# Kernel tuning notes

Hardware: AMD Instinct MI355X
Metric: run time of the kernel (lower is better)

## Reference

```python
import jax, jax.numpy as jnp
import numpy as np

V, S, D, H, L = 32000, 2048, 768, 12, 6
HD = D // H
EPS = 1e-5


def _sinusoidal_pe(s, d):
    pos = np.arange(s)[:, None].astype(np.float32)
    div = np.exp(np.arange(0, d, 2).astype(np.float32) * (-np.log(10000.0) / d))
    pe = np.zeros((s, d), dtype=np.float32)
    pe[:, 0::2] = np.sin(pos * div)
    pe[:, 1::2] = np.cos(pos * div)
    return jnp.asarray(pe)


def setup_inputs() -> dict:
    key = jax.random.key(0)
    ks = jax.random.split(key, 16)
    std = 0.02
    tok_emb = jax.random.normal(ks[0], (V, D), jnp.float32) * std
    tok_emb = tok_emb.at[1].set(0.0)  # padding_idx=1
    pos_enc = _sinusoidal_pe(S, D)
    attn_w = jax.random.normal(ks[1], (L, 3 * D, D), jnp.float32) * std
    attn_b = jnp.zeros((L, 3 * D), jnp.float32)
    proj_std = 0.02 / np.sqrt(2 * 6)
    proj_w = jax.random.normal(ks[2], (L, D, D), jnp.float32) * proj_std
    proj_b = jnp.zeros((L, D), jnp.float32)
    ln1_g = jnp.ones((L, D), jnp.float32); ln1_b = jnp.zeros((L, D), jnp.float32)
    ln2_g = jnp.ones((L, D), jnp.float32); ln2_b = jnp.zeros((L, D), jnp.float32)
    fc1_w = jax.random.normal(ks[3], (L, 4 * D, D), jnp.float32) * std
    fc1_b = jnp.zeros((L, 4 * D), jnp.float32)
    fc2_w = jax.random.normal(ks[4], (L, D, 4 * D), jnp.float32) * std
    fc2_b = jnp.zeros((L, D), jnp.float32)
    dec_w = jax.random.normal(ks[5], (V, D), jnp.float32) * std
    idx = jax.random.randint(ks[6], (2, S), 0, V)
    return dict(idx=idx, tok_emb=tok_emb, pos_enc=pos_enc, attn_w=attn_w,
                attn_b=attn_b, proj_w=proj_w, proj_b=proj_b, ln1_g=ln1_g,
                ln1_b=ln1_b, ln2_g=ln2_g, ln2_b=ln2_b, fc1_w=fc1_w,
                fc1_b=fc1_b, fc2_w=fc2_w, fc2_b=fc2_b, dec_w=dec_w)


def _ln(x, g, b):
    mu = jnp.mean(x, -1, keepdims=True)
    var = jnp.mean(jnp.square(x - mu), -1, keepdims=True)
    return (x - mu) * jax.lax.rsqrt(var + EPS) * g + b


def _forward(idx, tok_emb, pos_enc, attn_w, attn_b, proj_w, proj_b,
             ln1_g, ln1_b, ln2_g, ln2_b, fc1_w, fc1_b, fc2_w, fc2_b, dec_w):
    b, s = idx.shape
    x = tok_emb[idx] + pos_enc[:s]  # [b,s,d]
    for l in range(L):
        h = _ln(x, ln1_g[l], ln1_b[l])
        qkv = h @ attn_w[l].T + attn_b[l]
        q, k, v = jnp.split(qkv, 3, axis=-1)
        q = q.reshape(b, s, H, HD).transpose(0, 2, 1, 3)
        k = k.reshape(b, s, H, HD).transpose(0, 2, 1, 3)
        v = v.reshape(b, s, H, HD).transpose(0, 2, 1, 3)
        att = jnp.einsum('bhqd,bhkd->bhqk', q, k) * (1.0 / np.sqrt(HD))
        att = jax.nn.softmax(att, axis=-1)  # no causal mask in source
        y = jnp.einsum('bhqk,bhkd->bhqd', att, v)
        y = y.transpose(0, 2, 1, 3).reshape(b, s, D)
        x = x + (y @ proj_w[l].T + proj_b[l])
        h = _ln(x, ln2_g[l], ln2_b[l])
        h = jax.nn.gelu(h @ fc1_w[l].T + fc1_b[l])
        x = x + (h @ fc2_w[l].T + fc2_b[l])
    return x @ dec_w.T  # [b,s,V]


def reference(idx, tok_emb, pos_enc, attn_w, attn_b, proj_w, proj_b,
              ln1_g, ln1_b, ln2_g, ln2_b, fc1_w, fc1_b, fc2_w, fc2_b, dec_w):
    return _forward(idx, tok_emb, pos_enc, attn_w, attn_b, proj_w, proj_b,
                    ln1_g, ln1_b, ln2_g, ln2_b, fc1_w, fc1_b, fc2_w, fc2_b, dec_w)
```

## Files before the change

kernel.cpp:

```cpp
#include <hip/hip_runtime.h>
#include <hip/hip_bf16.h>
#include <stdint.h>


typedef unsigned short u16;
typedef __attribute__((ext_vector_type(8))) __bf16 bf16x8;
typedef __attribute__((ext_vector_type(4))) float f32x4;
typedef __attribute__((ext_vector_type(4))) unsigned int u32x4;
typedef __attribute__((ext_vector_type(4))) unsigned short u16x4;
typedef __attribute__((ext_vector_type(8))) unsigned short u16x8;

#define MFMA16(a, b, c) __builtin_amdgcn_mfma_f32_16x16x32_bf16((a), (b), (c), 0, 0, 0)

__device__ __forceinline__ float b2f(u16 u) {
  union { unsigned int i; float f; } x; x.i = ((unsigned int)u) << 16; return x.f;
}
__device__ __forceinline__ u16 f2b(float f) {
  union { float f; unsigned int i; } x; x.f = f;
  unsigned int r = x.i + 0x7fffu + ((x.i >> 16) & 1u);
  return (u16)(r >> 16);
}
__device__ __forceinline__ unsigned int cvtpk(float lo, float hi) {
  unsigned int r;
  asm("v_cvt_pk_bf16_f32 %0, %1, %2" : "=v"(r) : "v"(lo), "v"(hi));
  return r;
}
__device__ __forceinline__ float gelu_f(float v) {
  const float t = 0.7978845608028654f * (v + 0.044715f * v * v * v);
  const float e = __expf(-2.f * fabsf(t));
  float th = (1.f - e) / (1.f + e);
  th = (t < 0.f) ? -th : th;
  return 0.5f * v * (1.f + th);
}
__device__ __forceinline__ void lds16(u16* l, const u16* g) {
  __builtin_amdgcn_global_load_lds(
      (const __attribute__((address_space(1))) unsigned int*)g,
      (__attribute__((address_space(3))) unsigned int*)l, 16, 0, 0);
}

__global__ __launch_bounds__(256) void conv5_kernel(
    const float* __restrict__ s0, u16* __restrict__ d0, int n0,
    const float* __restrict__ s1, u16* __restrict__ d1, int n1,
    const float* __restrict__ s2, u16* __restrict__ d2, int n2,
    const float* __restrict__ s3, u16* __restrict__ d3, int n3,
    const float* __restrict__ s4, u16* __restrict__ d4, int n4) {
  const float* src; u16* dst; int n8;
  switch (blockIdx.y) {
    case 0: src = s0; dst = d0; n8 = n0; break;
    case 1: src = s1; dst = d1; n8 = n1; break;
    case 2: src = s2; dst = d2; n8 = n2; break;
    case 3: src = s3; dst = d3; n8 = n3; break;
    default: src = s4; dst = d4; n8 = n4; break;
  }
  int i = blockIdx.x * 256 + threadIdx.x;
  const int stride = gridDim.x * 256;
  for (; i < n8; i += stride) {
    const f32x4 a = *(const f32x4*)&src[(size_t)i * 8];
    const f32x4 b = *(const f32x4*)&src[(size_t)i * 8 + 4];
    u16x8 p;
#pragma unroll
    for (int j = 0; j < 4; ++j) { p[j] = f2b(a[j]); p[4 + j] = f2b(b[j]); }
    *(u16x8*)&dst[(size_t)i * 8] = p;
  }
}

__global__ __launch_bounds__(256) void convh_kernel(
    const float* __restrict__ src, u16* __restrict__ dst) {
  const int i = blockIdx.x * 256 + threadIdx.x;
  const f32x4 a = *(const f32x4*)&src[(size_t)i * 8];
  const f32x4 b = *(const f32x4*)&src[(size_t)i * 8 + 4];
  u16x8 p;
#pragma unroll
  for (int j = 0; j < 4; ++j) { p[j] = f2b(a[j]); p[4 + j] = f2b(b[j]); }
  *(u16x8*)&dst[(size_t)i * 8] = p;
}

__global__ __launch_bounds__(256) void embed_kernel(
    const int* __restrict__ idx, const float* __restrict__ tok,
    const float* __restrict__ pos, float* __restrict__ x) {
  const int t = blockIdx.x;
  const int s = t & 2047;
  const int tid = threadIdx.x;
  const size_t to = (size_t)idx[t] * 768;
  const size_t po = (size_t)s * 768;
  float* xr = x + (size_t)t * 768;
#pragma unroll
  for (int i = 0; i < 3; ++i) {
    const int d = tid + i * 256;
    xr[d] = tok[to + d] + pos[po + d];
  }
}

__global__ __launch_bounds__(256) void ln_kernel(
    const float* __restrict__ x, const float* __restrict__ g,
    const float* __restrict__ b, u16* __restrict__ out) {
  const int w = threadIdx.x >> 6, lane = threadIdx.x & 63;
  const int row = blockIdx.x * 4 + w;
  const float* xr = x + (size_t)row * 768;
  f32x4 v[3];
#pragma unroll
  for (int i = 0; i < 3; ++i) v[i] = *(const f32x4*)&xr[i * 256 + lane * 4];
  float s = 0.f;
#pragma unroll
  for (int i = 0; i < 3; ++i)
#pragma unroll
    for (int j = 0; j < 4; ++j) s += v[i][j];
#pragma unroll
  for (int m = 1; m < 64; m <<= 1) s += __shfl_xor(s, m);
  const float mu = s * (1.f / 768.f);
  float q = 0.f;
#pragma unroll
  for (int i = 0; i < 3; ++i)
#pragma unroll
    for (int j = 0; j < 4; ++j) {
      const float d = v[i][j] - mu;
      q += d * d;
    }
#pragma unroll
  for (int m = 1; m < 64; m <<= 1) q += __shfl_xor(q, m);
  const float rs = rsqrtf(q * (1.f / 768.f) + 1e-5f);
  u16* orow = out + (size_t)row * 768;
#pragma unroll
  for (int i = 0; i < 3; ++i) {
    const f32x4 gg = *(const f32x4*)&g[i * 256 + lane * 4];
    const f32x4 bb = *(const f32x4*)&b[i * 256 + lane * 4];
    u16x4 o;
#pragma unroll
    for (int j = 0; j < 4; ++j) o[j] = f2b((v[i][j] - mu) * rs * gg[j] + bb[j]);
    *(u16x4*)&orow[i * 256 + lane * 4] = o;
  }
}

template <int MODE, int MFAST, int SPLITK>
__global__ __launch_bounds__(256) void gemm_bb(
    const u16* __restrict__ A, const u16* __restrict__ B,
    const float* __restrict__ bias, u16* __restrict__ outb,
    float* __restrict__ outf, float* __restrict__ resid,
    u16* __restrict__ mirror, int N, int K) {
  __shared__ alignas(16) u16 As[2][128 * 64];
  __shared__ alignas(16) u16 Bs[2][128 * 64];
  const int tid = threadIdx.x;
  const int lane = tid & 63;
  const int w = tid >> 6;
  const int wr = (w >> 1) * 64;
  const int wc = (w & 1) * 64;
  const int fr = lane & 15;
  const int fg = lane >> 4;
  const int bn0 = (MFAST ? blockIdx.y : blockIdx.x) * 128;
  const int bm0 = (MFAST ? blockIdx.x : blockIdx.y) * 128;
  const int srow = tid >> 3;
  const int kseg = K / SPLITK;
  const int kbeg = (SPLITK > 1) ? blockIdx.z * kseg : 0;
  const int kend = kbeg + kseg;

  f32x4 acc[4][4] = {};

  auto stage = [&](int buf, int bk0) {
#pragma unroll
    for (int i = 0; i < 4; ++i) {
      const int row = i * 32 + srow;
      const int slot = (tid & 7) ^ (row & 7);
      lds16(&As[buf][(i * 256 + w * 64) * 8],
            &A[(size_t)(bm0 + row) * K + bk0 + slot * 8]);
      lds16(&Bs[buf][(i * 256 + w * 64) * 8],
            &B[(size_t)(bn0 + row) * K + bk0 + slot * 8]);
    }
  };

  stage(0, kbeg);
  int cur = 0;
  for (int bk0 = kbeg; bk0 < kend; bk0 += 64) {
    __syncthreads();
    if (bk0 + 64 < kend) stage(cur ^ 1, bk0 + 64);
#pragma unroll
    for (int kk = 0; kk < 64; kk += 32) {
      bf16x8 af[4], bfv[4];
#pragma unroll
      for (int m = 0; m < 4; ++m) {
        const int row = wr + m * 16 + fr;
        const int slot = ((kk >> 3) + fg) ^ (row & 7);
        af[m] = *(const bf16x8*)&As[cur][row * 64 + slot * 8];
      }
#pragma unroll
      for (int n = 0; n < 4; ++n) {
        const int row = wc + n * 16 + fr;
        const int slot = ((kk >> 3) + fg) ^ (row & 7);
        bfv[n] = *(const bf16x8*)&Bs[cur][row * 64 + slot * 8];
      }
#pragma unroll
      for (int m = 0; m < 4; ++m)
#pragma unroll
        for (int n = 0; n < 4; ++n)
          acc[m][n] = MFMA16(af[m], bfv[n], acc[m][n]);
    }
    cur ^= 1;
  }

  if (MODE == 4 && bn0 >= 1536) {
#pragma unroll
    for (int n = 0; n < 4; ++n) {
      const int col = bn0 + wc + n * 16 + fr;
      const float bv = bias[col];
      const int hcol = col - 1536;
      const size_t vbase =
          (size_t)(hcol >> 6) * 64 * 2048 + (size_t)(hcol & 63) * 2048;
#pragma unroll
      for (int m = 0; m < 4; ++m) {
        const int row0 = bm0 + wr + m * 16 + fg * 4;
        const size_t bboff = (size_t)(row0 >> 11) * 12 * 64 * 2048;
        const int s = row0 & 2047;
        u16x4 o;
#pragma unroll
        for (int r = 0; r < 4; ++r) o[r] = f2b(acc[m][n][r] + bv);
        *(u16x4*)&mirror[bboff + vbase + s] = o;
      }
    }
    return;
  }

#pragma unroll
  for (int n = 0; n < 4; ++n) {
    const int col = bn0 + wc + n * 16 + fr;
    const float bv =
        (bias && (SPLITK == 1 || blockIdx.z == 0)) ? bias[col] : 0.0f;
#pragma unroll
    for (int m = 0; m < 4; ++m) {
#pragma unroll
      for (int r = 0; r < 4; ++r) {
        const int row = bm0 + wr + m * 16 + fg * 4 + r;
        float v = acc[m][n][r] + bv;
        if (MODE == 1) v = gelu_f(v);
        const size_t off = (size_t)row * N + col;
        if (MODE == 2) {
          const float nv = resid[off] + v;
          resid[off] = nv;
          if (mirror) mirror[off] = f2b(nv);
        } else if (MODE == 5) {
          atomicAdd(&resid[off], v);
        } else if (MODE == 3) {
          __builtin_nontemporal_store(v, &outf[off]);
        } else {
          outb[off] = f2b(v);
        }
      }
    }
  }
}

#define G8PHASE(H, MH, LOADB)                                                 \
  {                                                                           \
    if (LOADB) {                                                              \
      _Pragma("unroll") for (int n = 0; n < 4; ++n) {                         \
        const int row = wn * 64 + n * 16 + fr;                                \
        bfv[n] = *(const bf16x8*)&Bs_[bufr * 16384 + (H) * 8192 + row * 32 +  \
                                      ((fg ^ ((row ^ (row >> 2)) & 3)) << 3)];\
      }                                                                       \
    }                                                                         \
    bf16x8 af[4];                                                             \
    _Pragma("unroll") for (int m = 0; m < 4; ++m) {                           \
      const int row = wm * 128 + (MH) * 64 + m * 16 + fr;                     \
      af[m] = *(const bf16x8*)&As_[bufr * 16384 + (H) * 8192 + row * 32 +     \
                                   ((fg ^ ((row ^ (row >> 2)) & 3)) << 3)];   \
    }                                                                         \
    __builtin_amdgcn_s_setprio(1);                                            \
    _Pragma("unroll") for (int m = 0; m < 4; ++m)                             \
      _Pragma("unroll") for (int n = 0; n < 4; ++n)                           \
        acc[(MH) * 4 + m][n] = MFMA16(af[m], bfv[n], acc[(MH) * 4 + m][n]);   \
    __builtin_amdgcn_s_setprio(0);                                            \
  }

template <int MODE, int MFAST>
__global__ __launch_bounds__(512, 2) void gemm8(
    const u16* __restrict__ A, const u16* __restrict__ B,
    const float* __restrict__ bias, u16* __restrict__ outb,
    float* __restrict__ outf, float* __restrict__ resid, int N, int K) {
  extern __shared__ u16 sm8[];
  u16* As_ = sm8;
  u16* Bs_ = sm8 + 32768;
  const int tid = threadIdx.x;
  const int lane = tid & 63;
  const int w = tid >> 6;
  const int wm = w >> 2;
  const int wn = w & 3;
  const int fr = lane & 15;
  const int fg = lane >> 4;
  const int bn0 = (MFAST ? blockIdx.y : blockIdx.x) * 256;
  const int bm0 = (MFAST ? blockIdx.x : blockIdx.y) * 256;
  const int nt = K >> 6;

  f32x4 acc[8][4] = {};
  bf16x8 bfv[4];

  auto stage = [&](u16* lbase, const u16* __restrict__ M, int rbase, int k0) {
#pragma unroll
    for (int i = 0; i < 2; ++i) {
      const int c = i * 512 + tid;
      const int row = c >> 2;
      const int slot = (c & 3) ^ ((row ^ (row >> 2)) & 3);
      lds16(lbase + (i * 512 + w * 64) * 8,
            M + (size_t)(rbase + row) * K + k0 + slot * 8);
    }
  };

  stage(As_ + 0, A, bm0, 0);
  stage(Bs_ + 0, B, bn0, 0);
  stage(As_ + 8192, A, bm0, 32);
  stage(Bs_ + 8192, B, bn0, 32);

  int bufr = 0;
  for (int t = 0; t < nt; ++t) {
    const int tn = (t + 1 < nt) ? t + 1 : t;
    const int bufw = bufr ^ 1;
    const int kn = tn * 64;
    asm volatile("s_waitcnt vmcnt(4)" ::: "memory");
    __builtin_amdgcn_sched_barrier(0);
    __builtin_amdgcn_s_barrier();
    stage(As_ + bufw * 16384, A, bm0, kn);
    G8PHASE(0, 0, true)
    stage(Bs_ + bufw * 16384, B, bn0, kn);
    G8PHASE(0, 1, false)
    asm volatile("s_waitcnt vmcnt(4)" ::: "memory");
    __builtin_amdgcn_sched_barrier(0);
    __builtin_amdgcn_s_barrier();
    stage(As_ + bufw * 16384 + 8192, A, bm0, kn + 32);
    G8PHASE(1, 0, true)
    stage(Bs_ + bufw * 16384 + 8192, B, bn0, kn + 32);
    G8PHASE(1, 1, false)
    bufr ^= 1;
  }

#pragma unroll
  for (int n = 0; n < 4; ++n) {
    const int col = bn0 + wn * 64 + n * 16 + fr;
    const float bv = bias ? bias[col] : 0.0f;
#pragma unroll
    for (int i = 0; i < 8; ++i) {
#pragma unroll
      for (int r = 0; r < 4; ++r) {
        const int row = bm0 + wm * 128 + i * 16 + fg * 4 + r;
        float v = acc[i][n][r] + bv;
        if (MODE == 1) v = gelu_f(v);
        const size_t off = (size_t)row * N + col;
        if (MODE == 2) {
          resid[off] += v;
        } else if (MODE == 3) {
          __builtin_nontemporal_store(v, &outf[off]);
        } else {
          outb[off] = f2b(v);
        }
      }
    }
  }
}

template <int MODE>
__global__ __launch_bounds__(256) void gemm_bt(
    const u16* __restrict__ A, const float* __restrict__ B,
    const float* __restrict__ bias, u16* __restrict__ outb,
    float* __restrict__ outf, float* __restrict__ resid,
    u16* __restrict__ mirror, int N, int K) {
  __shared__ alignas(16) u16 As[128 * 64];
  __shared__ alignas(16) u16 Bs[128 * 64];
  const int tid = threadIdx.x;
  const int lane = tid & 63;
  const int w = tid >> 6;
  const int wr = (w >> 1) * 64;
  const int wc = (w & 1) * 64;
  const int fr = lane & 15;
  const int fg = lane >> 4;
  const int bn0 = blockIdx.x * 128;
  const int bm0 = blockIdx.y * 128;

  f32x4 acc[4][4] = {};

  for (int bk0 = 0; bk0 < K; bk0 += 64) {
    __syncthreads();
#pragma unroll
    for (int i = 0; i < 4; ++i) {
      const int c = i * 256 + tid;
      const int row = c >> 3;
      const int e0 = (c & 7) * 8;
      *(u32x4*)&As[row * 64 + e0] =
          *(const u32x4*)&A[(size_t)(bm0 + row) * K + bk0 + e0];
    }
#pragma unroll
    for (int i = 0; i < 8; ++i) {
      const int c = i * 256 + tid;
      const int row = c >> 4;
      const int e0 = (c & 15) * 4;
      const f32x4 fv = *(const f32x4*)&B[(size_t)(bn0 + row) * K + bk0 + e0];
      u16x4 pv;
#pragma unroll
      for (int j = 0; j < 4; ++j) pv[j] = f2b(fv[j]);
      *(u16x4*)&Bs[row * 64 + e0] = pv;
    }
    __syncthreads();
#pragma unroll
    for (int kk = 0; kk < 64; kk += 32) {
      bf16x8 af[4], bfv[4];
#pragma unroll
      for (int m = 0; m < 4; ++m)
        af[m] = *(const bf16x8*)&As[(wr + m * 16 + fr) * 64 + kk + fg * 8];
#pragma unroll
      for (int n = 0; n < 4; ++n)
        bfv[n] = *(const bf16x8*)&Bs[(wc + n * 16 + fr) * 64 + kk + fg * 8];
#pragma unroll
      for (int m = 0; m < 4; ++m)
#pragma unroll
        for (int n = 0; n < 4; ++n)
          acc[m][n] = MFMA16(af[m], bfv[n], acc[m][n]);
    }
  }

#pragma unroll
  for (int n = 0; n < 4; ++n) {
    const int col = bn0 + wc + n * 16 + fr;
    const float bv = bias ? bias[col] : 0.0f;
#pragma unroll
    for (int m = 0; m < 4; ++m) {
#pragma unroll
      for (int r = 0; r < 4; ++r) {
        const int row = bm0 + wr + m * 16 + fg * 4 + r;
        float v = acc[m][n][r] + bv;
        if (MODE == 1) v = gelu_f(v);
        const size_t off = (size_t)row * N + col;
        if (MODE == 2) {
          const float nv = resid[off] + v;
          resid[off] = nv;
          if (mirror) mirror[off] = f2b(nv);
        } else if (MODE == 3) {
          __builtin_nontemporal_store(v, &outf[off]);
        } else {
          outb[off] = f2b(v);
        }
      }
    }
  }
}

__global__ __launch_bounds__(256) void vtrans_kernel(
    const u16* __restrict__ qkv, u16* __restrict__ vt) {
  __shared__ u16 tile[64][72];
  const int tid = threadIdx.x;
  const int s0 = blockIdx.x * 64;
  const int hh = blockIdx.y;
  const int bb = blockIdx.z;
  const size_t tb = (size_t)bb * 2048 * 2304;
#pragma unroll
  for (int i = 0; i < 2; ++i) {
    const int c = i * 256 + tid;
    const int sl = c >> 3;
    const int d0 = (c & 7) * 8;
    *(u16x8*)&tile[sl][d0] =
        *(const u16x8*)&qkv[tb + (size_t)(s0 + sl) * 2304 + 1536 + hh * 64 + d0];
  }
  __syncthreads();
  const size_t vtb = (size_t)((bb * 12 + hh) * 64) * 2048;
#pragma unroll
  for (int i = 0; i < 2; ++i) {
    const int c = i * 256 + tid;
    const int d = c >> 3;
    const int so = (c & 7) * 8;
    u16x8 p;
#pragma unroll
    for (int j = 0; j < 8; ++j) p[j] = tile[so + j][d];
    *(u16x8*)&vt[vtb + (size_t)d * 2048 + s0 + so] = p;
  }
}

__global__ __launch_bounds__(256) void attn_kernel(
    const u16* __restrict__ qkv, const u16* __restrict__ vt,
    u16* __restrict__ y) {
  __shared__ alignas(16) u16 Ks[2][64 * 64];
  __shared__ alignas(16) u16 VTs[2][64 * 64];
  __shared__ alignas(16) u16 Ps[4][16 * 64];
  const int tid = threadIdx.x;
  const int lane = tid & 63;
  const int w = tid >> 6;
  const int fr = lane & 15;
  const int fg = lane >> 4;
  const int hh = blockIdx.y;
  const int bb = blockIdx.z;
  const size_t tb = (size_t)bb * 2048 * 2304;
  const size_t vtb = (size_t)((bb * 12 + hh) * 64) * 2048;
  const int q0 = blockIdx.x * 64 + w * 16;

  const bf16x8 qf0 =
      *(const bf16x8*)&qkv[tb + (size_t)(q0 + fr) * 2304 + hh * 64 + fg * 8];
  const bf16x8 qf1 =
      *(const bf16x8*)&qkv[tb + (size_t)(q0 + fr) * 2304 + hh * 64 + 32 + fg * 8];

  f32x4 oacc[4] = {};
  float m = -INFINITY, l = 0.f;

  const int chunkrow = lane >> 3;
  const int chunkslot = lane & 7;

  auto stage = [&](int buf, int kt) {
#pragma unroll
    for (int i = 0; i < 2; ++i) {
      const int row = (i * 4 + w) * 8 + chunkrow;
      const int slot = chunkslot ^ (row & 7);
      lds16(&Ks[buf][(i * 4 + w) * 512],
            &qkv[tb + (size_t)(kt + row) * 2304 + 768 + hh * 64 + slot * 8]);
      lds16(&VTs[buf][(i * 4 + w) * 512],
            &vt[vtb + (size_t)row * 2048 + kt + slot * 8]);
    }
  };

  stage(0, 0);
  int cur = 0;
  for (int kt = 0; kt < 2048; kt += 64) {
    __syncthreads();
    if (kt + 64 < 2048) stage(cur ^ 1, kt + 64);

    f32x4 s[4] = {};
#pragma unroll
    for (int kb = 0; kb < 4; ++kb) {
      const int row = kb * 16 + fr;
      const int sl0 = (fg) ^ (row & 7);
      const int sl1 = (4 + fg) ^ (row & 7);
      const bf16x8 k0 = *(const bf16x8*)&Ks[cur][row * 64 + sl0 * 8];
      const bf16x8 k1 = *(const bf16x8*)&Ks[cur][row * 64 + sl1 * 8];
      s[kb] = MFMA16(k0, qf0, s[kb]);
      s[kb] = MFMA16(k1, qf1, s[kb]);
    }

    float v[4][4];
    float mx = -INFINITY;
#pragma unroll
    for (int kb = 0; kb < 4; ++kb)
#pragma unroll
      for (int r = 0; r < 4; ++r) {
        v[kb][r] = s[kb][r] * 0.125f;
        mx = fmaxf(mx, v[kb][r]);
      }
    mx = fmaxf(mx, __shfl_xor(mx, 16));
    mx = fmaxf(mx, __shfl_xor(mx, 32));

    float alpha = 1.f;
    const bool resc = !__all(mx <= m);
    if (resc) {
      const float mn = fmaxf(m, mx);
      alpha = __expf(m - mn);
      m = mn;
    }

    float ps = 0.f;
    unsigned int pk[4][2];
#pragma unroll
    for (int kb = 0; kb < 4; ++kb) {
      const float p0 = __expf(v[kb][0] - m);
      const float p1 = __expf(v[kb][1] - m);
      const float p2 = __expf(v[kb][2] - m);
      const float p3 = __expf(v[kb][3] - m);
      ps += (p0 + p1) + (p2 + p3);
      pk[kb][0] = cvtpk(p0, p1);
      pk[kb][1] = cvtpk(p2, p3);
    }
    ps += __shfl_xor(ps, 16);
    ps += __shfl_xor(ps, 32);
    l = l * alpha + ps;

#pragma unroll
    for (int kb = 0; kb < 4; ++kb)
#pragma unroll
      for (int h = 0; h < 2; ++h) {
        const int off = fr * 64 + (((2 * kb + (fg >> 1)) ^ (fr & 7)) << 3) +
                        (2 * (fg & 1) + h) * 2;
        *(unsigned int*)&Ps[w][off] = pk[kb][h];
      }

    if (resc) {
      float alq[4];
#pragma unroll
      for (int r = 0; r < 4; ++r) alq[r] = __shfl(alpha, fg * 4 + r);
#pragma unroll
      for (int db = 0; db < 4; ++db)
#pragma unroll
        for (int r = 0; r < 4; ++r) oacc[db][r] *= alq[r];
    }

#pragma unroll
    for (int kh = 0; kh < 2; ++kh) {
      const bf16x8 pa =
          *(const bf16x8*)&Ps[w][fr * 64 + (((kh * 4 + fg) ^ (fr & 7)) << 3)];
#pragma unroll
      for (int db = 0; db < 4; ++db) {
        const int row = db * 16 + fr;
        const int slot = (kh * 4 + fg) ^ (row & 7);
        const bf16x8 vb = *(const bf16x8*)&VTs[cur][row * 64 + slot * 8];
        oacc[db] = MFMA16(pa, vb, oacc[db]);
      }
    }
    cur ^= 1;
  }

  float rq[4];
#pragma unroll
  for (int r = 0; r < 4; ++r) rq[r] = 1.0f / __shfl(l, fg * 4 + r);
#pragma unroll
  for (int db = 0; db < 4; ++db) {
#pragma unroll
    for (int r = 0; r < 4; ++r) {
      const int row = q0 + fg * 4 + r;
      y[(size_t)(bb * 2048 + row) * 768 + hh * 64 + db * 16 + fr] =
          f2b(oacc[db][r] * rq[r]);
    }
  }
}

extern "C" void kernel_launch(void* const* d_in, const int* in_sizes, int n_in,
                              void* d_out, int out_size, void* d_ws,
                              size_t ws_size, hipStream_t stream) {
  const int*   idx   = (const int*)d_in[0];
  const float* tok   = (const float*)d_in[1];
  const float* pos   = (const float*)d_in[2];
  const float* attnw = (const float*)d_in[3];
  const float* attnb = (const float*)d_in[4];
  const float* projw = (const float*)d_in[5];
  const float* projb = (const float*)d_in[6];
  const float* ln1g  = (const float*)d_in[7];
  const float* ln1b  = (const float*)d_in[8];
  const float* ln2g  = (const float*)d_in[9];
  const float* ln2b  = (const float*)d_in[10];
  const float* fc1w  = (const float*)d_in[11];
  const float* fc1b  = (const float*)d_in[12];
  const float* fc2w  = (const float*)d_in[13];
  const float* fc2b  = (const float*)d_in[14];
  const float* decw  = (const float*)d_in[15];

  char* ws = (char*)d_ws;
  float* x = (float*)(ws);
  u16* h   = (u16*)(ws + 12582912);
  u16* qkv = (u16*)(ws + 18874368);
  u16* y   = (u16*)(ws + 37748736);
  u16* h2  = (u16*)(ws + 18874368);

  const size_t WB0 = 44040192;
  u16* attnw_b = (u16*)(ws + WB0);
  u16* projw_b = (u16*)(ws + WB0 + 21233664);
  u16* fc1w_b  = (u16*)(ws + WB0 + 28311552);
  u16* fc2w_b  = (u16*)(ws + WB0 + 56623104);
  u16* decw_b  = (u16*)(ws + WB0 + 84934656);
  u16* vt      = (u16*)(ws + WB0 + 84934656 + 49152000);
  const size_t NEED = WB0 + 84934656 + 49152000 + 12582912;

  embed_kernel<<<4096, 256, 0, stream>>>(idx, tok, pos, x);

  if (ws_size >= NEED) {
    conv5_kernel<<<dim3(1024, 5), 256, 0, stream>>>(
        attnw, attnw_b, 10616832 / 8, projw, projw_b, 3538944 / 8, fc1w,
        fc1w_b, 14155776 / 8, fc2w, fc2w_b, 14155776 / 8, decw, decw_b,
        24576000 / 8);

    for (int l = 0; l < 6; ++l) {
      ln_kernel<<<1024, 256, 0, stream>>>(x, ln1g + l * 768, ln1b + l * 768, h);
      gemm_bb<4, 0, 1><<<dim3(18, 32), 256, 0, stream>>>(
          h, attnw_b + (size_t)l * 2304 * 768, attnb + l * 2304, qkv, nullptr,
          nullptr, vt, 2304, 768);
      attn_kernel<<<dim3(32, 12, 2), 256, 0, stream>>>(qkv, vt, y);
      gemm_bb<5, 0, 2><<<dim3(6, 32, 2), 256, 0, stream>>>(
          y, projw_b + (size_t)l * 768 * 768, projb + l * 768, nullptr, nullptr,
          x, nullptr, 768, 768);
      ln_kernel<<<1024, 256, 0, stream>>>(x, ln2g + l * 768, ln2b + l * 768, h);
      gemm_bb<1, 0, 1><<<dim3(24, 32), 256, 0, stream>>>(
          h, fc1w_b + (size_t)l * 3072 * 768, fc1b + l * 3072, h2, nullptr,
          nullptr, nullptr, 3072, 768);
      gemm_bb<5, 0, 4><<<dim3(6, 32, 4), 256, 0, stream>>>(
          h2, fc2w_b + (size_t)l * 768 * 3072, fc2b + l * 768, nullptr, nullptr,
          x, nullptr, 768, 3072);
    }
    convh_kernel<<<1536, 256, 0, stream>>>(x, h);
    gemm8<3, 1><<<dim3(16, 125), 512, 131072, stream>>>(
        h, decw_b, nullptr, nullptr, (float*)d_out, nullptr, 32000, 768);
  } else {
    for (int l = 0; l < 6; ++l) {
      ln_kernel<<<1024, 256, 0, stream>>>(x, ln1g + l * 768, ln1b + l * 768, h);
      gemm_bt<0><<<dim3(18, 32), 256, 0, stream>>>(
          h, attnw + (size_t)l * 2304 * 768, attnb + l * 2304, qkv, nullptr,
          nullptr, nullptr, 2304, 768);
      vtrans_kernel<<<dim3(32, 12, 2), 256, 0, stream>>>(
          qkv, (u16*)(ws + 12582912));
      attn_kernel<<<dim3(32, 12, 2), 256, 0, stream>>>(
          qkv, (u16*)(ws + 12582912), y);
      gemm_bt<2><<<dim3(6, 32), 256, 0, stream>>>(
          y, projw + (size_t)l * 768 * 768, projb + l * 768, nullptr, nullptr,
          x, nullptr, 768, 768);
      ln_kernel<<<1024, 256, 0, stream>>>(x, ln2g + l * 768, ln2b + l * 768, h);
      gemm_bt<1><<<dim3(24, 32), 256, 0, stream>>>(
          h, fc1w + (size_t)l * 3072 * 768, fc1b + l * 3072, h2, nullptr,
          nullptr, nullptr, 3072, 768);
      gemm_bt<2><<<dim3(6, 32), 256, 0, stream>>>(
          h2, fc2w + (size_t)l * 768 * 3072, fc2b + l * 768, nullptr, nullptr,
          x, (l == 5) ? h : nullptr, 768, 3072);
    }
    gemm_bt<3><<<dim3(250, 32), 256, 0, stream>>>(
        h, decw, nullptr, nullptr, (float*)d_out, nullptr, nullptr, 32000, 768);
  }
}
```

Before: 1.761 ms.

## Add triple-buffered 256x128 GEMM kernel for QKV, FC1 and decoder

Adds a new 512-thread GEMM kernel with 256x128 tiles and a three-stage LDS ring that keeps two K tiles in flight, using explicit vmcnt waits and one barrier per tile. It replaces the 128x128 double-buffered GEMM for the QKV and FC1 projections and the 256x256 gemm8 kernel for the decoder projection. The aim is to hide global-load latency and raise MFMA utilisation through deeper prefetch. In exchange it uses 144KB of LDS per block, so only one block fits per CU, and the decoder now runs with smaller tiles and less reuse per block.

```diff
diff --git a/kernel.cpp b/kernel.cpp
--- a/kernel.cpp
+++ b/kernel.cpp
@@ -128,6 +128,152 @@
 #pragma unroll
     for (int j = 0; j < 4; ++j) o[j] = f2b((v[i][j] - mu) * rs * gg[j] + bb[j]);
     *(u16x4*)&orow[i * 256 + lane * 4] = o;
+  }
+}
+
+template <int MODE>
+__global__ __launch_bounds__(512, 1) void gemmW(
+    const u16* __restrict__ A, const u16* __restrict__ B,
+    const float* __restrict__ bias, u16* __restrict__ outb,
+    float* __restrict__ outf, u16* __restrict__ mirror, int N, int K) {
+  extern __shared__ u16 smw[];
+  const int tid = threadIdx.x;
+  const int lane = tid & 63;
+  const int w = tid >> 6;
+  const int wm = w >> 1;
+  const int wn = w & 1;
+  const int fr = lane & 15;
+  const int fg = lane >> 4;
+  const int bm0 = blockIdx.x * 256;
+  const int bn0 = blockIdx.y * 128;
+  const int nt = K >> 6;
+
+  f32x4 acc[4][4] = {};
+
+  auto stageT = [&](int buf, int t) {
+    const int k0 = t << 6;
+    u16* Ab = smw + buf * 24576;
+    u16* Bb = smw + buf * 24576 + 16384;
+#pragma unroll
+    for (int i = 0; i < 4; ++i) {
+      const int c = i * 512 + tid;
+      const int row = c >> 3;
+      const int slot = (c & 7) ^ (row & 7);
+      lds16(Ab + (i * 512 + w * 64) * 8,
+            A + (size_t)(bm0 + row) * K + k0 + slot * 8);
+    }
+#pragma unroll
+    for (int i = 0; i < 2; ++i) {
+      const int c = i * 512 + tid;
+      const int row = c >> 3;
+      const int slot = (c & 7) ^ (row & 7);
+      lds16(Bb + (i * 512 + w * 64) * 8,
+            B + (size_t)(bn0 + row) * K + k0 + slot * 8);
+    }
+  };
+
+  stageT(0, 0);
+  stageT(1, 1);
+  int buf = 0;
+  for (int t = 0; t < nt; ++t) {
+    if (t + 1 < nt)
+      asm volatile("s_waitcnt vmcnt(6)" ::: "memory");
+    else
+      asm volatile("s_waitcnt vmcnt(0)" ::: "memory");
+    __builtin_amdgcn_sched_barrier(0);
+    __builtin_amdgcn_s_barrier();
+    __builtin_amdgcn_sched_barrier(0);
+    if (t + 2 < nt) stageT((buf + 2) % 3, t + 2);
+    const u16* Ab = smw + buf * 24576;
+    const u16* Bb = smw + buf * 24576 + 16384;
+
+    bf16x8 af[2][4], bfv[2][2];
+#pragma unroll
+    for (int kx = 0; kx < 2; ++kx)
+#pragma unroll
+      for (int m = 0; m < 4; ++m) {
+        const int row = wm * 64 + m * 16 + fr;
+        const int slot = (kx * 4 + fg) ^ (row & 7);
+        af[kx][m] = *(const bf16x8*)&Ab[row * 64 + slot * 8];
+      }
+#pragma unroll
+    for (int kx = 0; kx < 2; ++kx)
+#pragma unroll
+      for (int n = 0; n < 2; ++n) {
+        const int row = wn * 64 + n * 16 + fr;
+        const int slot = (kx * 4 + fg) ^ (row & 7);
+        bfv[kx][n] = *(const bf16x8*)&Bb[row * 64 + slot * 8];
+      }
+    __builtin_amdgcn_s_setprio(1);
+#pragma unroll
+    for (int kx = 0; kx < 2; ++kx)
+#pragma unroll
+      for (int m = 0; m < 4; ++m)
+#pragma unroll
+        for (int n = 0; n < 2; ++n)
+          acc[m][n] = MFMA16(af[kx][m], bfv[kx][n], acc[m][n]);
+    __builtin_amdgcn_s_setprio(0);
+#pragma unroll
+    for (int kx = 0; kx < 2; ++kx)
+#pragma unroll
+      for (int n = 0; n < 2; ++n) {
+        const int row = wn * 64 + (2 + n) * 16 + fr;
+        const int slot = (kx * 4 + fg) ^ (row & 7);
+        bfv[kx][n] = *(const bf16x8*)&Bb[row * 64 + slot * 8];
+      }
+    __builtin_amdgcn_s_setprio(1);
+#pragma unroll
+    for (int kx = 0; kx < 2; ++kx)
+#pragma unroll
+      for (int m = 0; m < 4; ++m)
+#pragma unroll
+        for (int n = 0; n < 2; ++n)
+          acc[m][2 + n] = MFMA16(af[kx][m], bfv[kx][n], acc[m][2 + n]);
+    __builtin_amdgcn_s_setprio(0);
+    buf = (buf + 1) % 3;
+  }
+
+  if (MODE == 4 && bn0 >= 1536) {
+#pragma unroll
+    for (int n = 0; n < 4; ++n) {
+      const int col = bn0 + wn * 64 + n * 16 + fr;
+      const float bv = bias[col];
+      const int hcol = col - 1536;
+      const size_t vbase =
+          (size_t)(hcol >> 6) * 64 * 2048 + (size_t)(hcol & 63) * 2048;
+#pragma unroll
+      for (int m = 0; m < 4; ++m) {
+        const int row0 = bm0 + wm * 64 + m * 16 + fg * 4;
+        const size_t bboff = (size_t)(row0 >> 11) * 12 * 64 * 2048;
+        const int s = row0 & 2047;
+        u16x4 o;
+#pragma unroll
+        for (int r = 0; r < 4; ++r) o[r] = f2b(acc[m][n][r] + bv);
+        *(u16x4*)&mirror[bboff + vbase + s] = o;
+      }
+    }
+    return;
+  }
+
+#pragma unroll
+  for (int n = 0; n < 4; ++n) {
+    const int col = bn0 + wn * 64 + n * 16 + fr;
+    const float bv = bias ? bias[col] : 0.0f;
+#pragma unroll
+    for (int m = 0; m < 4; ++m) {
+#pragma unroll
+      for (int r = 0; r < 4; ++r) {
+        const int row = bm0 + wm * 64 + m * 16 + fg * 4 + r;
+        float v = acc[m][n][r] + bv;
+        if (MODE == 1) v = gelu_f(v);
+        const size_t off = (size_t)row * N + col;
+        if (MODE == 3) {
+          __builtin_nontemporal_store(v, &outf[off]);
+        } else {
+          outb[off] = f2b(v);
+        }
+      }
+    }
   }
 }
 
@@ -155,14 +301,14 @@
 
   f32x4 acc[4][4] = {};
 
-  auto stage = [&](int buf, int bk0) {
+  auto stage = [&](int bufq, int bk0) {
 #pragma unroll
     for (int i = 0; i < 4; ++i) {
       const int row = i * 32 + srow;
       const int slot = (tid & 7) ^ (row & 7);
-      lds16(&As[buf][(i * 256 + w * 64) * 8],
+      lds16(&As[bufq][(i * 256 + w * 64) * 8],
             &A[(size_t)(bm0 + row) * K + bk0 + slot * 8]);
-      lds16(&Bs[buf][(i * 256 + w * 64) * 8],
+      lds16(&Bs[bufq][(i * 256 + w * 64) * 8],
             &B[(size_t)(bn0 + row) * K + bk0 + slot * 8]);
     }
   };
@@ -194,28 +340,6 @@
           acc[m][n] = MFMA16(af[m], bfv[n], acc[m][n]);
     }
     cur ^= 1;
-  }
-
-  if (MODE == 4 && bn0 >= 1536) {
-#pragma unroll
-    for (int n = 0; n < 4; ++n) {
-      const int col = bn0 + wc + n * 16 + fr;
-      const float bv = bias[col];
-      const int hcol = col - 1536;
-      const size_t vbase =
-          (size_t)(hcol >> 6) * 64 * 2048 + (size_t)(hcol & 63) * 2048;
-#pragma unroll
-      for (int m = 0; m < 4; ++m) {
-        const int row0 = bm0 + wr + m * 16 + fg * 4;
-        const size_t bboff = (size_t)(row0 >> 11) * 12 * 64 * 2048;
-        const int s = row0 & 2047;
-        u16x4 o;
-#pragma unroll
-        for (int r = 0; r < 4; ++r) o[r] = f2b(acc[m][n][r] + bv);
-        *(u16x4*)&mirror[bboff + vbase + s] = o;
-      }
-    }
-    return;
   }
 
 #pragma unroll
@@ -237,112 +361,6 @@
           if (mirror) mirror[off] = f2b(nv);
         } else if (MODE == 5) {
           atomicAdd(&resid[off], v);
-        } else if (MODE == 3) {
-          __builtin_nontemporal_store(v, &outf[off]);
-        } else {
-          outb[off] = f2b(v);
-        }
-      }
-    }
-  }
-}
-
-#define G8PHASE(H, MH, LOADB)                                                 \
-  {                                                                           \
-    if (LOADB) {                                                              \
-      _Pragma("unroll") for (int n = 0; n < 4; ++n) {                         \
-        const int row = wn * 64 + n * 16 + fr;                                \
-        bfv[n] = *(const bf16x8*)&Bs_[bufr * 16384 + (H) * 8192 + row * 32 +  \
-                                      ((fg ^ ((row ^ (row >> 2)) & 3)) << 3)];\
-      }                                                                       \
-    }                                                                         \
-    bf16x8 af[4];                                                             \
-    _Pragma("unroll") for (int m = 0; m < 4; ++m) {                           \
-      const int row = wm * 128 + (MH) * 64 + m * 16 + fr;                     \
-      af[m] = *(const bf16x8*)&As_[bufr * 16384 + (H) * 8192 + row * 32 +     \
-                                   ((fg ^ ((row ^ (row >> 2)) & 3)) << 3)];   \
-    }                                                                         \
-    __builtin_amdgcn_s_setprio(1);                                            \
-    _Pragma("unroll") for (int m = 0; m < 4; ++m)                             \
-      _Pragma("unroll") for (int n = 0; n < 4; ++n)                           \
-        acc[(MH) * 4 + m][n] = MFMA16(af[m], bfv[n], acc[(MH) * 4 + m][n]);   \
-    __builtin_amdgcn_s_setprio(0);                                            \
-  }
-
-template <int MODE, int MFAST>
-__global__ __launch_bounds__(512, 2) void gemm8(
-    const u16* __restrict__ A, const u16* __restrict__ B,
-    const float* __restrict__ bias, u16* __restrict__ outb,
-    float* __restrict__ outf, float* __restrict__ resid, int N, int K) {
-  extern __shared__ u16 sm8[];
-  u16* As_ = sm8;
-  u16* Bs_ = sm8 + 32768;
-  const int tid = threadIdx.x;
-  const int lane = tid & 63;
-  const int w = tid >> 6;
-  const int wm = w >> 2;
-  const int wn = w & 3;
-  const int fr = lane & 15;
-  const int fg = lane >> 4;
-  const int bn0 = (MFAST ? blockIdx.y : blockIdx.x) * 256;
-  const int bm0 = (MFAST ? blockIdx.x : blockIdx.y) * 256;
-  const int nt = K >> 6;
-
-  f32x4 acc[8][4] = {};
-  bf16x8 bfv[4];
-
-  auto stage = [&](u16* lbase, const u16* __restrict__ M, int rbase, int k0) {
-#pragma unroll
-    for (int i = 0; i < 2; ++i) {
-      const int c = i * 512 + tid;
-      const int row = c >> 2;
-      const int slot = (c & 3) ^ ((row ^ (row >> 2)) & 3);
-      lds16(lbase + (i * 512 + w * 64) * 8,
-            M + (size_t)(rbase + row) * K + k0 + slot * 8);
-    }
-  };
-
-  stage(As_ + 0, A, bm0, 0);
-  stage(Bs_ + 0, B, bn0, 0);
-  stage(As_ + 8192, A, bm0, 32);
-  stage(Bs_ + 8192, B, bn0, 32);
-
-  int bufr = 0;
-  for (int t = 0; t < nt; ++t) {
-    const int tn = (t + 1 < nt) ? t + 1 : t;
-    const int bufw = bufr ^ 1;
-    const int kn = tn * 64;
-    asm volatile("s_waitcnt vmcnt(4)" ::: "memory");
-    __builtin_amdgcn_sched_barrier(0);
-    __builtin_amdgcn_s_barrier();
-    stage(As_ + bufw * 16384, A, bm0, kn);
-    G8PHASE(0, 0, true)
-    stage(Bs_ + bufw * 16384, B, bn0, kn);
-    G8PHASE(0, 1, false)
-    asm volatile("s_waitcnt vmcnt(4)" ::: "memory");
-    __builtin_amdgcn_sched_barrier(0);
-    __builtin_amdgcn_s_barrier();
-    stage(As_ + bufw * 16384 + 8192, A, bm0, kn + 32);
-    G8PHASE(1, 0, true)
-    stage(Bs_ + bufw * 16384 + 8192, B, bn0, kn + 32);
-    G8PHASE(1, 1, false)
-    bufr ^= 1;
-  }
-
-#pragma unroll
-  for (int n = 0; n < 4; ++n) {
-    const int col = bn0 + wn * 64 + n * 16 + fr;
-    const float bv = bias ? bias[col] : 0.0f;
-#pragma unroll
-    for (int i = 0; i < 8; ++i) {
-#pragma unroll
-      for (int r = 0; r < 4; ++r) {
-        const int row = bm0 + wm * 128 + i * 16 + fg * 4 + r;
-        float v = acc[i][n][r] + bv;
-        if (MODE == 1) v = gelu_f(v);
-        const size_t off = (size_t)row * N + col;
-        if (MODE == 2) {
-          resid[off] += v;
         } else if (MODE == 3) {
           __builtin_nontemporal_store(v, &outf[off]);
         } else {
@@ -496,14 +514,14 @@
   const int chunkrow = lane >> 3;
   const int chunkslot = lane & 7;
 
-  auto stage = [&](int buf, int kt) {
+  auto stage = [&](int bufq, int kt) {
 #pragma unroll
     for (int i = 0; i < 2; ++i) {
       const int row = (i * 4 + w) * 8 + chunkrow;
       const int slot = chunkslot ^ (row & 7);
-      lds16(&Ks[buf][(i * 4 + w) * 512],
+      lds16(&Ks[bufq][(i * 4 + w) * 512],
             &qkv[tb + (size_t)(kt + row) * 2304 + 768 + hh * 64 + slot * 8]);
-      lds16(&VTs[buf][(i * 4 + w) * 512],
+      lds16(&VTs[bufq][(i * 4 + w) * 512],
             &vt[vtb + (size_t)row * 2048 + kt + slot * 8]);
     }
   };
@@ -656,23 +674,23 @@
 
     for (int l = 0; l < 6; ++l) {
       ln_kernel<<<1024, 256, 0, stream>>>(x, ln1g + l * 768, ln1b + l * 768, h);
-      gemm_bb<4, 0, 1><<<dim3(18, 32), 256, 0, stream>>>(
+      gemmW<4><<<dim3(16, 18), 512, 147456, stream>>>(
           h, attnw_b + (size_t)l * 2304 * 768, attnb + l * 2304, qkv, nullptr,
-          nullptr, vt, 2304, 768);
+          vt, 2304, 768);
       attn_kernel<<<dim3(32, 12, 2), 256, 0, stream>>>(qkv, vt, y);
       gemm_bb<5, 0, 2><<<dim3(6, 32, 2), 256, 0, stream>>>(
           y, projw_b + (size_t)l * 768 * 768, projb + l * 768, nullptr, nullptr,
           x, nullptr, 768, 768);
       ln_kernel<<<1024, 256, 0, stream>>>(x, ln2g + l * 768, ln2b + l * 768, h);
-      gemm_bb<1, 0, 1><<<dim3(24, 32), 256, 0, stream>>>(
+      gemmW<1><<<dim3(16, 24), 512, 147456, stream>>>(
           h, fc1w_b + (size_t)l * 3072 * 768, fc1b + l * 3072, h2, nullptr,
-          nullptr, nullptr, 3072, 768);
+          nullptr, 3072, 768);
       gemm_bb<5, 0, 4><<<dim3(6, 32, 4), 256, 0, stream>>>(
           h2, fc2w_b + (size_t)l * 768 * 3072, fc2b + l * 768, nullptr, nullptr,
           x, nullptr, 768, 3072);
     }
     convh_kernel<<<1536, 256, 0, stream>>>(x, h);
-    gemm8<3, 1><<<dim3(16, 125), 512, 131072, stream>>>(
+    gemmW<3><<<dim3(16, 250), 512, 147456, stream>>>(
         h, decw_b, nullptr, nullptr, (float*)d_out, nullptr, 32000, 768);
   } else {
     for (int l = 0; l < 6; ++l) {
```

Result: no change. 1.769 ms (+0.4%).
